# Kernel tuning notes

Hardware: AMD Instinct MI355X
Metric: run time of the kernel (lower is better)

## Reference

```python
import jax, jax.numpy as jnp
import numpy as np

GRID_NUM = 3  # pykan 'grid' (number of intervals)
K = 3         # spline order

def bspline_basis(x, grid, k):
    # Cox-de Boor recursion, matching pykan B_batch with a shared extended grid.
    # x: (N, Din); grid: (G,) extended grid with G = GRID_NUM + 2*k + 1
    x = x[..., None]  # (N, Din, 1)
    B = ((x >= grid[:-1]) & (x < grid[1:])).astype(x.dtype)  # (N, Din, G-1)
    for p in range(1, k + 1):
        left = (x - grid[:-(p + 1)]) / (grid[p:-1] - grid[:-(p + 1)])
        right = (grid[p + 1:] - x) / (grid[p + 1:] - grid[1:-p])
        B = left * B[..., :-1] + right * B[..., 1:]
    return B  # (N, Din, GRID_NUM + k)

def setup_inputs() -> dict:
    key = jax.random.key(0)
    k1, k2, k3 = jax.random.split(key, 3)
    Bsz, S, Din, Dout = 4, 2048, 768, 768
    x = jax.random.normal(k1, (Bsz, S, Din), dtype=jnp.float32)
    # noise-scale-like init for spline coefficients (noise_scale=0.1)
    coef = (0.1 / GRID_NUM) * jax.random.normal(k2, (Dout, Din, GRID_NUM + K), dtype=jnp.float32)
    inv_sqrt_in = np.float32(1.0 / np.sqrt(Din))
    scale_base = inv_sqrt_in + 0.1 * inv_sqrt_in * jax.random.normal(k3, (Dout, Din), dtype=jnp.float32)
    scale_sp = jnp.ones((Dout, Din), dtype=jnp.float32)
    bias = jnp.zeros((Dout,), dtype=jnp.float32)
    return {"x": x, "coef": coef, "scale_base": scale_base, "scale_sp": scale_sp, "bias": bias}

def reference(x, coef, scale_base, scale_sp, bias):
    # x: (B, S, Din) -> flatten tokens as the original module does
    Bsz, S, Din = x.shape
    xf = x.reshape(-1, Din)  # (N, Din)
    # extended grid: linspace(-1,1,GRID_NUM+1) extended by K points each side (h = 2/GRID_NUM)
    h = 2.0 / GRID_NUM
    grid = jnp.arange(-K, GRID_NUM + K + 1, dtype=x.dtype) * h - 1.0  # (GRID_NUM + 2K + 1,)
    basis = bspline_basis(xf, grid, K)  # (N, Din, GRID_NUM+K)
    # per-edge activation: scale_base*silu(x) + scale_sp*spline(x); mask==1; symbolic branch==0
    base = jax.nn.silu(xf) @ scale_base.T  # (N, Dout)
    spline = jnp.einsum('nim,oim->no', basis, scale_sp[:, :, None] * coef)  # (N, Dout)
    out = base + spline + bias  # bias from pykan biases[l].weight
    return out.reshape(Bsz, S, -1)
```

## Files before the change

### kernel.cpp

```cpp
#include <hip/hip_runtime.h>


typedef _Float16 f16;
typedef __attribute__((ext_vector_type(4))) _Float16 f16x4;
typedef __attribute__((ext_vector_type(8))) _Float16 f16x8;
typedef __attribute__((ext_vector_type(4))) float f32x4;

#define NTOK 8192
#define DIN 768
#define DOUT 768
#define KAUG 5376
#define BM 128
#define BN 192
#define BK 64
#define NKT (KAUG / BK)
#define ASZ (BM * BK)
#define BSZ (BN * BK)
#define NBLK ((NTOK / BM) * (DOUT / BN))

typedef __attribute__((address_space(1))) void gvoid;
typedef __attribute__((address_space(3))) void lvoid;

__device__ __forceinline__ void spline6(float xv, float* __restrict__ B, float& s) {
  s = xv / (1.0f + __expf(-xv));
  const float h = 2.0f / 3.0f;
  float Bb[9];
#pragma unroll
  for (int g = 0; g < 9; ++g) {
    float t0 = (float)(g - 3) * h - 1.0f;
    float t1 = (float)(g - 2) * h - 1.0f;
    Bb[g] = (xv >= t0 && xv < t1) ? 1.0f : 0.0f;
  }
#pragma unroll
  for (int p = 1; p <= 3; ++p) {
    float inv = 1.0f / ((float)p * h);
#pragma unroll
    for (int j = 0; j < 8; ++j) {
      if (j < 9 - p) {
        float tj = (float)(j - 3) * h - 1.0f;
        float tjp1 = (float)(j + p + 1 - 3) * h - 1.0f;
        Bb[j] = (xv - tj) * inv * Bb[j] + (tjp1 - xv) * inv * Bb[j + 1];
      }
    }
  }
#pragma unroll
  for (int m = 0; m < 6; ++m) B[m] = Bb[m];
}

#define NBLK_A ((NTOK * DIN) / 2048)
#define NBLK_W ((DOUT * DIN) / 1024)

__global__ __launch_bounds__(256) void build_AW(const float* __restrict__ x,
                                                const float* __restrict__ sb,
                                                const float* __restrict__ ssp,
                                                const float* __restrict__ coef,
                                                f16* __restrict__ Aa,
                                                f16* __restrict__ Wa) {
  const int b = blockIdx.x;
  if (b < NBLK_A) {
    int idx = (b * 256 + threadIdx.x) * 8;
    float4 x0 = *(const float4*)(x + idx);
    float4 x1 = *(const float4*)(x + idx + 4);
    float xs[8] = {x0.x, x0.y, x0.z, x0.w, x1.x, x1.y, x1.z, x1.w};
    int n = idx / DIN;
    int i = idx - n * DIN;

    float Bv[8][6], sv[8];
#pragma unroll
    for (int t = 0; t < 8; ++t) spline6(xs[t], Bv[t], sv[t]);

    size_t base = (size_t)n * KAUG + i;
    f16x8 s8;
#pragma unroll
    for (int t = 0; t < 8; ++t) s8[t] = (f16)sv[t];
    *(f16x8*)(Aa + base) = s8;
#pragma unroll
    for (int m = 0; m < 6; ++m) {
      f16x8 b8;
#pragma unroll
      for (int t = 0; t < 8; ++t) b8[t] = (f16)Bv[t][m];
      *(f16x8*)(Aa + base + (size_t)(m + 1) * DIN) = b8;
    }
  } else {
    int idx = ((b - NBLK_A) * 256 + threadIdx.x) * 4;
    float4 bb = *(const float4*)(sb + idx);
    float4 pp = *(const float4*)(ssp + idx);
    int o = idx / DIN;
    int i = idx - o * DIN;
    size_t base = (size_t)o * KAUG + i;
    f16x4 w0 = {(f16)bb.x, (f16)bb.y, (f16)bb.z, (f16)bb.w};
    *(f16x4*)(Wa + base) = w0;
    float c[24];
#pragma unroll
    for (int j = 0; j < 6; ++j) {
      float4 cv = *(const float4*)(coef + (size_t)idx * 6 + j * 4);
      c[j * 4 + 0] = cv.x; c[j * 4 + 1] = cv.y; c[j * 4 + 2] = cv.z; c[j * 4 + 3] = cv.w;
    }
    float sp[4] = {pp.x, pp.y, pp.z, pp.w};
#pragma unroll
    for (int m = 0; m < 6; ++m) {
      f16x4 wv = {(f16)(sp[0] * c[0 * 6 + m]), (f16)(sp[1] * c[1 * 6 + m]),
                  (f16)(sp[2] * c[2 * 6 + m]), (f16)(sp[3] * c[3 * 6 + m])};
      *(f16x4*)(Wa + base + (size_t)(m + 1) * DIN) = wv;
    }
  }
}

__global__ __launch_bounds__(512, 2) void kan_gemm(const f16* __restrict__ A,
                                                   const f16* __restrict__ W,
                                                   const float* __restrict__ bias,
                                                   float* __restrict__ out) {
  __shared__ alignas(16) f16 As[3 * ASZ];
  __shared__ alignas(16) f16 Bs[3 * BSZ];

  const int tid = threadIdx.x;
  const int wave = tid >> 6;
  const int lane = tid & 63;

  const int bid = blockIdx.x;
  const int wg = (bid & 7) * (NBLK / 8) + (bid >> 3);
  const int m0 = (wg >> 2) * BM;
  const int n0 = (wg & 3) * BN;

  const int wm = (wave >> 2) * 64;
  const int wn = (wave & 3) * 48;
  const int r = lane & 15;
  const int q = lane >> 4;
  const int r7 = r & 7;

  f32x4 acc[4][3] = {};

  const int cA0 = tid, cA1 = tid + 512;
  const int cB0 = tid, cB1 = tid + 512, cB2 = tid + 1024;
  const f16* gA0 = A + (size_t)(m0 + (cA0 >> 3)) * KAUG + ((cA0 & 7) ^ ((cA0 >> 3) & 7)) * 8;
  const f16* gA1 = A + (size_t)(m0 + (cA1 >> 3)) * KAUG + ((cA1 & 7) ^ ((cA1 >> 3) & 7)) * 8;
  const f16* gB0 = W + (size_t)(n0 + (cB0 >> 3)) * KAUG + ((cB0 & 7) ^ ((cB0 >> 3) & 7)) * 8;
  const f16* gB1 = W + (size_t)(n0 + (cB1 >> 3)) * KAUG + ((cB1 & 7) ^ ((cB1 >> 3) & 7)) * 8;
  const f16* gB2 = W + (size_t)(n0 + (cB2 >> 3)) * KAUG + ((cB2 & 7) ^ ((cB2 >> 3) & 7)) * 8;
  const int dA0 = wave * 512, dA1 = 4096 + wave * 512;
  const int dB0 = wave * 512, dB1 = 4096 + wave * 512, dB2 = 8192 + wave * 512;

#define STAGE_B(bufi, kt)                                                                  \
  do {                                                                                     \
    const int ko = (kt)*BK;                                                                \
    f16* bb_ = Bs + (bufi)*BSZ;                                                            \
    __builtin_amdgcn_global_load_lds((gvoid*)(gB0 + ko), (lvoid*)(bb_ + dB0), 16, 0, 0);   \
    __builtin_amdgcn_global_load_lds((gvoid*)(gB1 + ko), (lvoid*)(bb_ + dB1), 16, 0, 0);   \
    __builtin_amdgcn_global_load_lds((gvoid*)(gB2 + ko), (lvoid*)(bb_ + dB2), 16, 0, 0);   \
  } while (0)

#define STAGE_A(bufi, kt)                                                                  \
  do {                                                                                     \
    const int ko = (kt)*BK;                                                                \
    f16* ab_ = As + (bufi)*ASZ;                                                            \
    __builtin_amdgcn_global_load_lds((gvoid*)(gA0 + ko), (lvoid*)(ab_ + dA0), 16, 0, 0);   \
    __builtin_amdgcn_global_load_lds((gvoid*)(gA1 + ko), (lvoid*)(ab_ + dA1), 16, 0, 0);   \
  } while (0)

#define PH(bufi, kh, STAGE_STMT)                                                           \
  do {                                                                                     \
    const f16* Ab = As + (bufi)*ASZ;                                                       \
    const f16* Bb = Bs + (bufi)*BSZ;                                                       \
    const int sl = (((kh)*4 + q) ^ r7) * 8;                                                \
    f16x8 af[4], bf[3];                                                                    \
    _Pragma("unroll") for (int mi = 0; mi < 4; ++mi) af[mi] =                              \
        *(const f16x8*)&Ab[(wm + mi * 16 + r) * BK + sl];                                  \
    _Pragma("unroll") for (int ni = 0; ni < 3; ++ni) bf[ni] =                              \
        *(const f16x8*)&Bb[(wn + ni * 16 + r) * BK + sl];                                  \
    STAGE_STMT;                                                                            \
    __builtin_amdgcn_s_setprio(1);                                                         \
    _Pragma("unroll") for (int mi = 0; mi < 4; ++mi)                                       \
        _Pragma("unroll") for (int ni = 0; ni < 3; ++ni) acc[mi][ni] =                     \
        __builtin_amdgcn_mfma_f32_16x16x32_f16(af[mi], bf[ni], acc[mi][ni], 0, 0, 0);      \
    __builtin_amdgcn_s_setprio(0);                                                         \
  } while (0)

#define FENCE_BAR(VMC)                                            \
  do {                                                            \
    asm volatile("s_waitcnt lgkmcnt(0) vmcnt(" #VMC ")" ::: "memory"); \
    __builtin_amdgcn_sched_barrier(0);                            \
    __builtin_amdgcn_s_barrier();                                 \
  } while (0)

#define MID_BAR()                                                 \
  do {                                                            \
    asm volatile("s_waitcnt lgkmcnt(0)" ::: "memory");            \
    __builtin_amdgcn_sched_barrier(0);                            \
    __builtin_amdgcn_s_barrier();                                 \
  } while (0)

  STAGE_B(0, 0);
  STAGE_A(0, 0);
  STAGE_B(1, 1);
  STAGE_A(1, 1);
  FENCE_BAR(5);

  for (int t = 0; t < NKT - 2; ++t) {
    const int rb = t % 3;
    const int pb = (t + 2) % 3;
    PH(rb, 0, STAGE_B(pb, t + 2));
    MID_BAR();
    PH(rb, 1, STAGE_A(pb, t + 2));
    FENCE_BAR(5);
  }
  {
    const int rb = (NKT - 2) % 3;
    PH(rb, 0, (void)0);
    MID_BAR();
    PH(rb, 1, (void)0);
    FENCE_BAR(0);
  }
  {
    const int rb = (NKT - 1) % 3;
    PH(rb, 0, (void)0);
    PH(rb, 1, (void)0);
  }

#undef STAGE_A
#undef STAGE_B
#undef PH
#undef FENCE_BAR
#undef MID_BAR

#pragma unroll
  for (int mi = 0; mi < 4; ++mi) {
#pragma unroll
    for (int ni = 0; ni < 3; ++ni) {
      const int gcol = n0 + wn + ni * 16 + r;
      const float bv = bias[gcol];
#pragma unroll
      for (int rg = 0; rg < 4; ++rg) {
        const int grow = m0 + wm + mi * 16 + q * 4 + rg;
        out[(size_t)grow * DOUT + gcol] = acc[mi][ni][rg] + bv;
      }
    }
  }
}

extern "C" void kernel_launch(void* const* d_in, const int* in_sizes, int n_in,
                              void* d_out, int out_size, void* d_ws, size_t ws_size,
                              hipStream_t stream) {
  const float* x = (const float*)d_in[0];
  const float* coef = (const float*)d_in[1];
  const float* scale_base = (const float*)d_in[2];
  const float* scale_sp = (const float*)d_in[3];
  const float* bias = (const float*)d_in[4];
  float* out = (float*)d_out;

  f16* Aa = (f16*)d_ws;
  f16* Wa = (f16*)((char*)d_ws + (size_t)NTOK * KAUG * 2);

  build_AW<<<NBLK_A + NBLK_W, 256, 0, stream>>>(x, scale_base, scale_sp, coef, Aa, Wa);
  kan_gemm<<<NBLK, 512, 0, stream>>>(Aa, Wa, bias, out);
}
```

Measured before the change: 191.0 us.

## Fuse operand build and GEMM into one cooperative kernel with grid sync

New measurement: 321.7 us. 68.4% more time.

```diff
diff --git a/kernel.cpp b/kernel.cpp
--- a/kernel.cpp
+++ b/kernel.cpp
@@ -1,8 +1,8 @@
 #include <hip/hip_runtime.h>
+#include <hip/hip_cooperative_groups.h>
 
 
 typedef _Float16 f16;
-typedef __attribute__((ext_vector_type(4))) _Float16 f16x4;
 typedef __attribute__((ext_vector_type(8))) _Float16 f16x8;
 typedef __attribute__((ext_vector_type(4))) float f32x4;
 
@@ -17,6 +17,9 @@
 #define ASZ (BM * BK)
 #define BSZ (BN * BK)
 #define NBLK ((NTOK / BM) * (DOUT / BN))
+#define NTHR (NBLK * 512)
+#define A_CHUNKS ((NTOK * DIN) / 8)
+#define W_CHUNKS ((DOUT * DIN) / 8)
 
 typedef __attribute__((address_space(1))) void gvoid;
 typedef __attribute__((address_space(3))) void lvoid;
@@ -47,29 +50,35 @@
   for (int m = 0; m < 6; ++m) B[m] = Bb[m];
 }
 
-#define NBLK_A ((NTOK * DIN) / 2048)
-#define NBLK_W ((DOUT * DIN) / 1024)
-
-__global__ __launch_bounds__(256) void build_AW(const float* __restrict__ x,
-                                                const float* __restrict__ sb,
-                                                const float* __restrict__ ssp,
-                                                const float* __restrict__ coef,
-                                                f16* __restrict__ Aa,
-                                                f16* __restrict__ Wa) {
-  const int b = blockIdx.x;
-  if (b < NBLK_A) {
-    int idx = (b * 256 + threadIdx.x) * 8;
+__global__ __launch_bounds__(512, 2) void kan_fused(const float* __restrict__ x,
+                                                    const float* __restrict__ sb,
+                                                    const float* __restrict__ ssp,
+                                                    const float* __restrict__ coef,
+                                                    const float* __restrict__ bias,
+                                                    f16* __restrict__ Aa,
+                                                    f16* __restrict__ Wa,
+                                                    float* __restrict__ out) {
+  __shared__ alignas(16) f16 As[3 * ASZ];
+  __shared__ alignas(16) f16 Bs[3 * BSZ];
+
+  const int tid = threadIdx.x;
+  const int bid = blockIdx.x;
+  const int gtid = bid * 512 + tid;
+
+#pragma unroll 1
+  for (int it = 0; it < 6; ++it) {
+    const int idx = (gtid + it * NTHR) * 8;
     float4 x0 = *(const float4*)(x + idx);
     float4 x1 = *(const float4*)(x + idx + 4);
     float xs[8] = {x0.x, x0.y, x0.z, x0.w, x1.x, x1.y, x1.z, x1.w};
-    int n = idx / DIN;
-    int i = idx - n * DIN;
+    const int n = idx / DIN;
+    const int i = idx - n * DIN;
 
     float Bv[8][6], sv[8];
 #pragma unroll
     for (int t = 0; t < 8; ++t) spline6(xs[t], Bv[t], sv[t]);
 
-    size_t base = (size_t)n * KAUG + i;
+    const size_t base = (size_t)n * KAUG + i;
     f16x8 s8;
 #pragma unroll
     for (int t = 0; t < 8; ++t) s8[t] = (f16)sv[t];
@@ -81,43 +90,43 @@
       for (int t = 0; t < 8; ++t) b8[t] = (f16)Bv[t][m];
       *(f16x8*)(Aa + base + (size_t)(m + 1) * DIN) = b8;
     }
-  } else {
-    int idx = ((b - NBLK_A) * 256 + threadIdx.x) * 4;
-    float4 bb = *(const float4*)(sb + idx);
-    float4 pp = *(const float4*)(ssp + idx);
-    int o = idx / DIN;
-    int i = idx - o * DIN;
-    size_t base = (size_t)o * KAUG + i;
-    f16x4 w0 = {(f16)bb.x, (f16)bb.y, (f16)bb.z, (f16)bb.w};
-    *(f16x4*)(Wa + base) = w0;
-    float c[24];
-#pragma unroll
-    for (int j = 0; j < 6; ++j) {
+  }
+  if (gtid < W_CHUNKS) {
+    const int idx = gtid * 8;
+    float4 b0 = *(const float4*)(sb + idx);
+    float4 b1 = *(const float4*)(sb + idx + 4);
+    float4 p0 = *(const float4*)(ssp + idx);
+    float4 p1 = *(const float4*)(ssp + idx + 4);
+    float bs[8] = {b0.x, b0.y, b0.z, b0.w, b1.x, b1.y, b1.z, b1.w};
+    float ps[8] = {p0.x, p0.y, p0.z, p0.w, p1.x, p1.y, p1.z, p1.w};
+    const int o = idx / DIN;
+    const int i = idx - o * DIN;
+    float c[48];
+#pragma unroll
+    for (int j = 0; j < 12; ++j) {
       float4 cv = *(const float4*)(coef + (size_t)idx * 6 + j * 4);
       c[j * 4 + 0] = cv.x; c[j * 4 + 1] = cv.y; c[j * 4 + 2] = cv.z; c[j * 4 + 3] = cv.w;
     }
-    float sp[4] = {pp.x, pp.y, pp.z, pp.w};
+    const size_t base = (size_t)o * KAUG + i;
+    f16x8 w8;
+#pragma unroll
+    for (int t = 0; t < 8; ++t) w8[t] = (f16)bs[t];
+    *(f16x8*)(Wa + base) = w8;
 #pragma unroll
     for (int m = 0; m < 6; ++m) {
-      f16x4 wv = {(f16)(sp[0] * c[0 * 6 + m]), (f16)(sp[1] * c[1 * 6 + m]),
-                  (f16)(sp[2] * c[2 * 6 + m]), (f16)(sp[3] * c[3 * 6 + m])};
-      *(f16x4*)(Wa + base + (size_t)(m + 1) * DIN) = wv;
-    }
-  }
-}
-
-__global__ __launch_bounds__(512, 2) void kan_gemm(const f16* __restrict__ A,
-                                                   const f16* __restrict__ W,
-                                                   const float* __restrict__ bias,
-                                                   float* __restrict__ out) {
-  __shared__ alignas(16) f16 As[3 * ASZ];
-  __shared__ alignas(16) f16 Bs[3 * BSZ];
-
-  const int tid = threadIdx.x;
+      f16x8 v;
+#pragma unroll
+      for (int t = 0; t < 8; ++t) v[t] = (f16)(ps[t] * c[t * 6 + m]);
+      *(f16x8*)(Wa + base + (size_t)(m + 1) * DIN) = v;
+    }
+  }
+
+  __threadfence();
+  cooperative_groups::this_grid().sync();
+
   const int wave = tid >> 6;
   const int lane = tid & 63;
 
-  const int bid = blockIdx.x;
   const int wg = (bid & 7) * (NBLK / 8) + (bid >> 3);
   const int m0 = (wg >> 2) * BM;
   const int n0 = (wg & 3) * BN;
@@ -132,11 +141,11 @@
 
   const int cA0 = tid, cA1 = tid + 512;
   const int cB0 = tid, cB1 = tid + 512, cB2 = tid + 1024;
-  const f16* gA0 = A + (size_t)(m0 + (cA0 >> 3)) * KAUG + ((cA0 & 7) ^ ((cA0 >> 3) & 7)) * 8;
-  const f16* gA1 = A + (size_t)(m0 + (cA1 >> 3)) * KAUG + ((cA1 & 7) ^ ((cA1 >> 3) & 7)) * 8;
-  const f16* gB0 = W + (size_t)(n0 + (cB0 >> 3)) * KAUG + ((cB0 & 7) ^ ((cB0 >> 3) & 7)) * 8;
-  const f16* gB1 = W + (size_t)(n0 + (cB1 >> 3)) * KAUG + ((cB1 & 7) ^ ((cB1 >> 3) & 7)) * 8;
-  const f16* gB2 = W + (size_t)(n0 + (cB2 >> 3)) * KAUG + ((cB2 & 7) ^ ((cB2 >> 3) & 7)) * 8;
+  const f16* gA0 = Aa + (size_t)(m0 + (cA0 >> 3)) * KAUG + ((cA0 & 7) ^ ((cA0 >> 3) & 7)) * 8;
+  const f16* gA1 = Aa + (size_t)(m0 + (cA1 >> 3)) * KAUG + ((cA1 & 7) ^ ((cA1 >> 3) & 7)) * 8;
+  const f16* gB0 = Wa + (size_t)(n0 + (cB0 >> 3)) * KAUG + ((cB0 & 7) ^ ((cB0 >> 3) & 7)) * 8;
+  const f16* gB1 = Wa + (size_t)(n0 + (cB1 >> 3)) * KAUG + ((cB1 & 7) ^ ((cB1 >> 3) & 7)) * 8;
+  const f16* gB2 = Wa + (size_t)(n0 + (cB2 >> 3)) * KAUG + ((cB2 & 7) ^ ((cB2 >> 3) & 7)) * 8;
   const int dA0 = wave * 512, dA1 = 4096 + wave * 512;
   const int dB0 = wave * 512, dB1 = 4096 + wave * 512, dB2 = 8192 + wave * 512;
 
@@ -175,11 +184,11 @@
     __builtin_amdgcn_s_setprio(0);                                                         \
   } while (0)
 
-#define FENCE_BAR(VMC)                                            \
-  do {                                                            \
+#define FENCE_BAR(VMC)                                                 \
+  do {                                                                 \
     asm volatile("s_waitcnt lgkmcnt(0) vmcnt(" #VMC ")" ::: "memory"); \
-    __builtin_amdgcn_sched_barrier(0);                            \
-    __builtin_amdgcn_s_barrier();                                 \
+    __builtin_amdgcn_sched_barrier(0);                                 \
+    __builtin_amdgcn_s_barrier();                                      \
   } while (0)
 
 #define MID_BAR()                                                 \
@@ -250,6 +259,7 @@
   f16* Aa = (f16*)d_ws;
   f16* Wa = (f16*)((char*)d_ws + (size_t)NTOK * KAUG * 2);
 
-  build_AW<<<NBLK_A + NBLK_W, 256, 0, stream>>>(x, scale_base, scale_sp, coef, Aa, Wa);
-  kan_gemm<<<NBLK, 512, 0, stream>>>(Aa, Wa, bias, out);
+  void* args[] = {(void*)&x, (void*)&scale_base, (void*)&scale_sp, (void*)&coef,
+                  (void*)&bias, (void*)&Aa, (void*)&Wa, (void*)&out};
+  hipLaunchCooperativeKernel((void*)kan_fused, dim3(NBLK), dim3(512), args, 0, stream);
 }
```

## Shrink GEMM tile to 128x96 with 4 waves and asymmetric A/B buffering

Applied to the files above, without the earlier changes.

Result: slower. 195.0 us (+2.1%).

```diff
diff --git a/kernel.cpp b/kernel.cpp
--- a/kernel.cpp
+++ b/kernel.cpp
@@ -2,7 +2,6 @@
 
 
 typedef _Float16 f16;
-typedef __attribute__((ext_vector_type(4))) _Float16 f16x4;
 typedef __attribute__((ext_vector_type(8))) _Float16 f16x8;
 typedef __attribute__((ext_vector_type(4))) float f32x4;
 
@@ -11,7 +10,7 @@
 #define DOUT 768
 #define KAUG 5376
 #define BM 128
-#define BN 192
+#define BN 96
 #define BK 64
 #define NKT (KAUG / BK)
 #define ASZ (BM * BK)
@@ -88,8 +87,9 @@
     int o = idx / DIN;
     int i = idx - o * DIN;
     size_t base = (size_t)o * KAUG + i;
-    f16x4 w0 = {(f16)bb.x, (f16)bb.y, (f16)bb.z, (f16)bb.w};
-    *(f16x4*)(Wa + base) = w0;
+    typedef __attribute__((ext_vector_type(4))) _Float16 f16x4_t;
+    f16x4_t w0 = {(f16)bb.x, (f16)bb.y, (f16)bb.z, (f16)bb.w};
+    *(f16x4_t*)(Wa + base) = w0;
     float c[24];
 #pragma unroll
     for (int j = 0; j < 6; ++j) {
@@ -99,18 +99,18 @@
     float sp[4] = {pp.x, pp.y, pp.z, pp.w};
 #pragma unroll
     for (int m = 0; m < 6; ++m) {
-      f16x4 wv = {(f16)(sp[0] * c[0 * 6 + m]), (f16)(sp[1] * c[1 * 6 + m]),
-                  (f16)(sp[2] * c[2 * 6 + m]), (f16)(sp[3] * c[3 * 6 + m])};
-      *(f16x4*)(Wa + base + (size_t)(m + 1) * DIN) = wv;
-    }
-  }
-}
-
-__global__ __launch_bounds__(512, 2) void kan_gemm(const f16* __restrict__ A,
-                                                   const f16* __restrict__ W,
-                                                   const float* __restrict__ bias,
-                                                   float* __restrict__ out) {
-  __shared__ alignas(16) f16 As[3 * ASZ];
+      f16x4_t wv = {(f16)(sp[0] * c[0 * 6 + m]), (f16)(sp[1] * c[1 * 6 + m]),
+                    (f16)(sp[2] * c[2 * 6 + m]), (f16)(sp[3] * c[3 * 6 + m])};
+      *(f16x4_t*)(Wa + base + (size_t)(m + 1) * DIN) = wv;
+    }
+  }
+}
+
+__global__ __launch_bounds__(256) void kan_gemm(const f16* __restrict__ A,
+                                                const f16* __restrict__ W,
+                                                const float* __restrict__ bias,
+                                                float* __restrict__ out) {
+  __shared__ alignas(16) f16 As[2 * ASZ];
   __shared__ alignas(16) f16 Bs[3 * BSZ];
 
   const int tid = threadIdx.x;
@@ -119,67 +119,60 @@
 
   const int bid = blockIdx.x;
   const int wg = (bid & 7) * (NBLK / 8) + (bid >> 3);
-  const int m0 = (wg >> 2) * BM;
-  const int n0 = (wg & 3) * BN;
-
-  const int wm = (wave >> 2) * 64;
-  const int wn = (wave & 3) * 48;
+  const int m0 = (wg >> 3) * BM;
+  const int n0 = (wg & 7) * BN;
+
+  const int wm = (wave >> 1) * 64;
+  const int wn = (wave & 1) * 48;
   const int r = lane & 15;
   const int q = lane >> 4;
   const int r7 = r & 7;
 
   f32x4 acc[4][3] = {};
 
-  const int cA0 = tid, cA1 = tid + 512;
-  const int cB0 = tid, cB1 = tid + 512, cB2 = tid + 1024;
-  const f16* gA0 = A + (size_t)(m0 + (cA0 >> 3)) * KAUG + ((cA0 & 7) ^ ((cA0 >> 3) & 7)) * 8;
-  const f16* gA1 = A + (size_t)(m0 + (cA1 >> 3)) * KAUG + ((cA1 & 7) ^ ((cA1 >> 3) & 7)) * 8;
-  const f16* gB0 = W + (size_t)(n0 + (cB0 >> 3)) * KAUG + ((cB0 & 7) ^ ((cB0 >> 3) & 7)) * 8;
-  const f16* gB1 = W + (size_t)(n0 + (cB1 >> 3)) * KAUG + ((cB1 & 7) ^ ((cB1 >> 3) & 7)) * 8;
-  const f16* gB2 = W + (size_t)(n0 + (cB2 >> 3)) * KAUG + ((cB2 & 7) ^ ((cB2 >> 3) & 7)) * 8;
-  const int dA0 = wave * 512, dA1 = 4096 + wave * 512;
-  const int dB0 = wave * 512, dB1 = 4096 + wave * 512, dB2 = 8192 + wave * 512;
-
-#define STAGE_B(bufi, kt)                                                                  \
-  do {                                                                                     \
-    const int ko = (kt)*BK;                                                                \
-    f16* bb_ = Bs + (bufi)*BSZ;                                                            \
-    __builtin_amdgcn_global_load_lds((gvoid*)(gB0 + ko), (lvoid*)(bb_ + dB0), 16, 0, 0);   \
-    __builtin_amdgcn_global_load_lds((gvoid*)(gB1 + ko), (lvoid*)(bb_ + dB1), 16, 0, 0);   \
-    __builtin_amdgcn_global_load_lds((gvoid*)(gB2 + ko), (lvoid*)(bb_ + dB2), 16, 0, 0);   \
-  } while (0)
-
-#define STAGE_A(bufi, kt)                                                                  \
-  do {                                                                                     \
-    const int ko = (kt)*BK;                                                                \
-    f16* ab_ = As + (bufi)*ASZ;                                                            \
-    __builtin_amdgcn_global_load_lds((gvoid*)(gA0 + ko), (lvoid*)(ab_ + dA0), 16, 0, 0);   \
-    __builtin_amdgcn_global_load_lds((gvoid*)(gA1 + ko), (lvoid*)(ab_ + dA1), 16, 0, 0);   \
-  } while (0)
-
-#define PH(bufi, kh, STAGE_STMT)                                                           \
-  do {                                                                                     \
-    const f16* Ab = As + (bufi)*ASZ;                                                       \
-    const f16* Bb = Bs + (bufi)*BSZ;                                                       \
-    const int sl = (((kh)*4 + q) ^ r7) * 8;                                                \
-    f16x8 af[4], bf[3];                                                                    \
-    _Pragma("unroll") for (int mi = 0; mi < 4; ++mi) af[mi] =                              \
-        *(const f16x8*)&Ab[(wm + mi * 16 + r) * BK + sl];                                  \
-    _Pragma("unroll") for (int ni = 0; ni < 3; ++ni) bf[ni] =                              \
-        *(const f16x8*)&Bb[(wn + ni * 16 + r) * BK + sl];                                  \
-    STAGE_STMT;                                                                            \
-    __builtin_amdgcn_s_setprio(1);                                                         \
-    _Pragma("unroll") for (int mi = 0; mi < 4; ++mi)                                       \
-        _Pragma("unroll") for (int ni = 0; ni < 3; ++ni) acc[mi][ni] =                     \
-        __builtin_amdgcn_mfma_f32_16x16x32_f16(af[mi], bf[ni], acc[mi][ni], 0, 0, 0);      \
-    __builtin_amdgcn_s_setprio(0);                                                         \
-  } while (0)
-
-#define FENCE_BAR(VMC)                                            \
-  do {                                                            \
-    asm volatile("s_waitcnt lgkmcnt(0) vmcnt(" #VMC ")" ::: "memory"); \
-    __builtin_amdgcn_sched_barrier(0);                            \
-    __builtin_amdgcn_s_barrier();                                 \
+  const f16* gA[4];
+  const f16* gB[3];
+#pragma unroll
+  for (int j = 0; j < 4; ++j) {
+    const int c = tid + j * 256;
+    gA[j] = A + (size_t)(m0 + (c >> 3)) * KAUG + (((c & 7) ^ ((c >> 3) & 7)) * 8);
+  }
+#pragma unroll
+  for (int j = 0; j < 3; ++j) {
+    const int c = tid + j * 256;
+    gB[j] = W + (size_t)(n0 + (c >> 3)) * KAUG + (((c & 7) ^ ((c >> 3) & 7)) * 8);
+  }
+
+#define STAGE_A(bufi, kt)                                                                \
+  do {                                                                                   \
+    const int ko = (kt)*BK;                                                              \
+    f16* ab_ = As + (bufi)*ASZ + wave * 512;                                             \
+    _Pragma("unroll") for (int j = 0; j < 4; ++j)                                        \
+        __builtin_amdgcn_global_load_lds((gvoid*)(gA[j] + ko),                           \
+                                         (lvoid*)(ab_ + j * 2048), 16, 0, 0);            \
+  } while (0)
+
+#define STAGE_B(bufi, kt)                                                                \
+  do {                                                                                   \
+    const int ko = (kt)*BK;                                                              \
+    f16* bb_ = Bs + (bufi)*BSZ + wave * 512;                                             \
+    _Pragma("unroll") for (int j = 0; j < 3; ++j)                                        \
+        __builtin_amdgcn_global_load_lds((gvoid*)(gB[j] + ko),                           \
+                                         (lvoid*)(bb_ + j * 2048), 16, 0, 0);            \
+  } while (0)
+
+#define PH(Ab, Bb, kh, STAGE_STMT)                                                       \
+  do {                                                                                   \
+    const int sl = (((kh)*4 + q) ^ r7) * 8;                                              \
+    f16x8 af[4], bf[3];                                                                  \
+    _Pragma("unroll") for (int mi = 0; mi < 4; ++mi) af[mi] =                            \
+        *(const f16x8*)&(Ab)[(wm + mi * 16 + r) * BK + sl];                              \
+    _Pragma("unroll") for (int ni = 0; ni < 3; ++ni) bf[ni] =                            \
+        *(const f16x8*)&(Bb)[(wn + ni * 16 + r) * BK + sl];                              \
+    STAGE_STMT;                                                                          \
+    _Pragma("unroll") for (int mi = 0; mi < 4; ++mi)                                     \
+        _Pragma("unroll") for (int ni = 0; ni < 3; ++ni) acc[mi][ni] =                   \
+        __builtin_amdgcn_mfma_f32_16x16x32_f16(af[mi], bf[ni], acc[mi][ni], 0, 0, 0);    \
   } while (0)
 
 #define MID_BAR()                                                 \
@@ -189,38 +182,47 @@
     __builtin_amdgcn_s_barrier();                                 \
   } while (0)
 
+#define FENCE_BAR(VMC)                                                 \
+  do {                                                                 \
+    asm volatile("s_waitcnt lgkmcnt(0) vmcnt(" #VMC ")" ::: "memory"); \
+    __builtin_amdgcn_sched_barrier(0);                                 \
+    __builtin_amdgcn_s_barrier();                                      \
+  } while (0)
+
+  STAGE_A(0, 0);
   STAGE_B(0, 0);
-  STAGE_A(0, 0);
   STAGE_B(1, 1);
-  STAGE_A(1, 1);
-  FENCE_BAR(5);
-
-  for (int t = 0; t < NKT - 2; ++t) {
-    const int rb = t % 3;
-    const int pb = (t + 2) % 3;
-    PH(rb, 0, STAGE_B(pb, t + 2));
+  asm volatile("s_waitcnt vmcnt(3)" ::: "memory");
+  __builtin_amdgcn_sched_barrier(0);
+  __builtin_amdgcn_s_barrier();
+
+  for (int t = 0; t < NKT; ++t) {
+    const f16* Ab = As + (t & 1) * ASZ;
+    const f16* Bb = Bs + (t % 3) * BSZ;
+
+    if (t + 1 < NKT) {
+      PH(Ab, Bb, 0, STAGE_A((t + 1) & 1, t + 1));
+    } else {
+      PH(Ab, Bb, 0, (void)0);
+    }
     MID_BAR();
-    PH(rb, 1, STAGE_A(pb, t + 2));
-    FENCE_BAR(5);
-  }
-  {
-    const int rb = (NKT - 2) % 3;
-    PH(rb, 0, (void)0);
-    MID_BAR();
-    PH(rb, 1, (void)0);
-    FENCE_BAR(0);
-  }
-  {
-    const int rb = (NKT - 1) % 3;
-    PH(rb, 0, (void)0);
-    PH(rb, 1, (void)0);
+
+    if (t + 2 < NKT) {
+      PH(Ab, Bb, 1, STAGE_B((t + 2) % 3, t + 2));
+      FENCE_BAR(3);
+    } else if (t + 1 < NKT) {
+      PH(Ab, Bb, 1, (void)0);
+      FENCE_BAR(0);
+    } else {
+      PH(Ab, Bb, 1, (void)0);
+    }
   }
 
 #undef STAGE_A
 #undef STAGE_B
 #undef PH
+#undef MID_BAR
 #undef FENCE_BAR
-#undef MID_BAR
 
 #pragma unroll
   for (int mi = 0; mi < 4; ++mi) {
@@ -251,5 +253,5 @@
   f16* Wa = (f16*)((char*)d_ws + (size_t)NTOK * KAUG * 2);
 
   build_AW<<<NBLK_A + NBLK_W, 256, 0, stream>>>(x, scale_base, scale_sp, coef, Aa, Wa);
-  kan_gemm<<<NBLK, 512, 0, stream>>>(Aa, Wa, bias, out);
-}
+  kan_gemm<<<NBLK, 256, 0, stream>>>(Aa, Wa, bias, out);
+}
```
